# Optimization experiments

Measured on AMD Instinct MI355X. Metric: run time of the kernel, lower is better.

## Reference

```python
import jax, jax.numpy as jnp
import numpy as np

B, T, N, D = 4, 12, 10000, 2
E = 320000
H = 64          # encoder_embed_dim
K = 2           # Chebyshev diffusion steps
P = 1           # pred_node_dim
NPRED = 12      # n_pred


def _xavier(key, shape):
    fan_in, fan_out = shape[-2], shape[-1]
    limit = np.sqrt(6.0 / (fan_in + fan_out)).astype(np.float32)
    return jax.random.uniform(key, shape, jnp.float32, -limit, limit)


def setup_inputs() -> dict:
    key = jax.random.key(0)
    ks = jax.random.split(key, 8)
    x = jax.random.normal(ks[0], (B, T, N, D), jnp.float32)
    edge_index = jax.random.randint(ks[1], (2, E), 0, N, dtype=jnp.int64)
    # positive diffusion weights, scaled ~1/avg_degree for numerical sanity
    edge_attr = jax.random.uniform(ks[2], (E,), jnp.float32) * 0.03
    W0 = _xavier(ks[3], (K, D + H, H))   # layer 0: in = node_feat + H
    b0 = jnp.zeros((H,), jnp.float32)
    W1 = _xavier(ks[4], (K, 2 * H, H))   # layer 1: in = H + H
    b1 = jnp.zeros((H,), jnp.float32)
    Wp = _xavier(ks[5], (H, P))
    bp = jnp.zeros((P,), jnp.float32)
    return {"x": x, "edge_index": edge_index, "edge_attr": edge_attr,
            "W0": W0, "b0": b0, "W1": W1, "b1": b1, "Wp": Wp, "bp": bp}


def dcrnn_layer(x, h, src, dst, ew, W, b):
    # x: [B,N,Dx], h: [B,N,H]; inp: [B,N,C] with C = Dx + H
    inp = jnp.concatenate([x, h], axis=-1)
    out = jnp.einsum('bnc,co->bno', inp, W[0])
    Hc = inp
    for k in range(1, W.shape[0]):
        # propagate: message = norm * x_j (gather at src), scatter-add at dst
        msg = ew[None, :, None] * Hc[:, src]          # [B,E,C]
        Hc = jnp.zeros_like(Hc).at[:, dst].add(msg)   # [B,N,C]
        out = out + jnp.einsum('bnc,co->bno', Hc, W[k])
    return out + b


def reference(x, edge_index, edge_attr, W0, b0, W1, b1, Wp, bp):
    src, dst = edge_index[0], edge_index[1]
    Bs, Ts, Ns, _ = x.shape
    h0 = jnp.zeros((Bs, Ns, H), x.dtype)

    def step(h, x_t):
        # layer 0: input features + recurrent state
        h1 = jax.nn.relu(dcrnn_layer(x_t, h, src, dst, edge_attr, W0, b0))
        # layer 1: x_b = h_b after layer 0, so both halves are h1
        h2 = jax.nn.relu(dcrnn_layer(h1, h1, src, dst, edge_attr, W1, b1))
        return h2, None

    xs = jnp.swapaxes(x, 0, 1)  # [T,B,N,D]
    h, _ = jax.lax.scan(step, h0, xs)
    out = h @ Wp + bp                                  # [B,N,P]
    # unsqueeze(1).repeat(1, n_pred, 1, 1)
    return jnp.broadcast_to(out[:, None], (Bs, NPRED, Ns, out.shape[-1]))
```

## Files before the change

### kernel.cpp

```cpp
#include <hip/hip_runtime.h>

#define BB 4
#define TT 12
#define NN 10000
#define DD 2
#define EE 320000
#define HH 64
#define NPREDD 12
#define TD 24
#define CAP 512

typedef __attribute__((ext_vector_type(8))) short bf16x8;
typedef __attribute__((ext_vector_type(4))) float f32x4;
typedef unsigned short u16;

__device__ __forceinline__ unsigned int pack2(float lo, float hi) {
    unsigned int r;
    asm("v_cvt_pk_bf16_f32 %0, %1, %2" : "=v"(r) : "v"(lo), "v"(hi));
    return r;
}
__device__ __forceinline__ float b2f(u16 u) {
    return __uint_as_float(((unsigned)u) << 16);
}

__global__ void hist_kernel(const int* __restrict__ dstv, int* __restrict__ deg) {
    int e = blockIdx.x*256 + threadIdx.x;
    if (e < EE) atomicAdd(&deg[dstv[e]], 1);
}

__global__ void scan_kernel(const int* __restrict__ deg, int* __restrict__ row_ptr,
                            int* __restrict__ cursor) {
    __shared__ int part[1024];
    int tid = threadIdx.x;
    const int CH = 10;
    int start = tid*CH;
    int s = 0;
    if (start < NN)
        for (int i=0;i<CH;i++) s += deg[start+i];
    part[tid] = s;
    __syncthreads();
    if (tid == 0) {
        int acc = 0;
        for (int i=0;i<1024;i++){ int v=part[i]; part[i]=acc; acc+=v; }
        row_ptr[NN] = acc;
    }
    __syncthreads();
    if (start < NN) {
        int acc = part[tid];
        for (int i=0;i<CH;i++){ int idx=start+i; row_ptr[idx]=acc; cursor[idx]=acc; acc+=deg[idx]; }
    }
}

__global__ void fill_kernel(const int* __restrict__ srcv, const int* __restrict__ dstv,
                            const float* __restrict__ ew, int* __restrict__ cursor,
                            int2* __restrict__ csr) {
    int e = blockIdx.x*256 + threadIdx.x;
    if (e < EE) {
        int d = dstv[e];
        int pos = atomicAdd(&cursor[d], 1);
        csr[pos] = make_int2(srcv[e], __float_as_int(ew[e]));
    }
}

__global__ void transpose_x(const float* __restrict__ x, float* __restrict__ xTb) {
    int idx = blockIdx.x*256 + threadIdx.x;
    if (idx >= BB*TT*NN*DD) return;
    int d = idx & 1;
    int n = (idx >> 1) % NN;
    int t = (idx / (NN*DD)) % TT;
    int b = idx / (TT*NN*DD);
    xTb[((size_t)n*TD + (t*DD + d))*BB + b] = x[idx];
}

__global__ __launch_bounds__(256)
void ax_gather(const float* __restrict__ xTb, const int* __restrict__ row_ptr,
               const int2* __restrict__ csr, float* __restrict__ AXb) {
    int gw = (blockIdx.x*256 + threadIdx.x) >> 6;
    if (gw >= NN) return;
    int n = gw;
    int lane = threadIdx.x & 63;
    int half = lane >> 5;
    int c = lane & 31;
    float4 acc = {0.f,0.f,0.f,0.f};
    int e0 = row_ptr[n], e1 = row_ptr[n+1];
    for (int e = e0; e < e1; e += 8) {
        int ia = e + half, ib = e + 2 + half, ic = e + 4 + half, id = e + 6 + half;
        int2 ca = csr[ia]; int2 cb = csr[ib]; int2 cc = csr[ic]; int2 cd = csr[id];
        float wa = (ia < e1) ? __int_as_float(ca.y) : 0.f;
        float wb = (ib < e1) ? __int_as_float(cb.y) : 0.f;
        float wc = (ic < e1) ? __int_as_float(cc.y) : 0.f;
        float wd = (id < e1) ? __int_as_float(cd.y) : 0.f;
        const float4 va = *(const float4*)(xTb + (size_t)ca.x*(TD*BB) + c*4);
        const float4 vb = *(const float4*)(xTb + (size_t)cb.x*(TD*BB) + c*4);
        const float4 vc = *(const float4*)(xTb + (size_t)cc.x*(TD*BB) + c*4);
        const float4 vd = *(const float4*)(xTb + (size_t)cd.x*(TD*BB) + c*4);
        acc.x = fmaf(wa, va.x, acc.x); acc.y = fmaf(wa, va.y, acc.y);
        acc.z = fmaf(wa, va.z, acc.z); acc.w = fmaf(wa, va.w, acc.w);
        acc.x = fmaf(wb, vb.x, acc.x); acc.y = fmaf(wb, vb.y, acc.y);
        acc.z = fmaf(wb, vb.z, acc.z); acc.w = fmaf(wb, vb.w, acc.w);
        acc.x = fmaf(wc, vc.x, acc.x); acc.y = fmaf(wc, vc.y, acc.y);
        acc.z = fmaf(wc, vc.z, acc.z); acc.w = fmaf(wc, vc.w, acc.w);
        acc.x = fmaf(wd, vd.x, acc.x); acc.y = fmaf(wd, vd.y, acc.y);
        acc.z = fmaf(wd, vd.z, acc.z); acc.w = fmaf(wd, vd.w, acc.w);
    }
    acc.x += __shfl_xor(acc.x, 32); acc.y += __shfl_xor(acc.y, 32);
    acc.z += __shfl_xor(acc.z, 32); acc.w += __shfl_xor(acc.w, 32);
    if (lane < TD) *(float4*)(AXb + (size_t)n*(TD*BB) + lane*4) = acc;
}

__global__ void prep_wfrag(const float* __restrict__ W0, const float* __restrict__ W1,
                           unsigned short* __restrict__ wf0, unsigned short* __restrict__ wf1) {
    int tid = blockIdx.x*256 + threadIdx.x;
    if (tid >= 2560) return;
    int layer = tid / 1280;
    int r = tid % 1280;
    int lane = r & 63;
    int ctkt = r >> 6;
    int ct = ctkt / 5, kt = ctkt % 5;
    int c = ct*16 + (lane & 15);
    int k0 = kt*32 + (lane >> 4)*8;
    unsigned short* dst = (layer ? wf1 : wf0) + r*8;
    for (int j=0;j<8;j++) {
        int k = k0 + j;
        float w = 0.f;
        if (layer == 0) {
            if (k < 64)        w = W0[(2+k)*64 + c];
            else if (k < 128)  w = W0[4224 + (2+(k-64))*64 + c];
            else if (k == 128) w = W0[c];
            else if (k == 129) w = W0[64 + c];
            else if (k == 130) w = W0[4224 + c];
            else if (k == 131) w = W0[4224 + 64 + c];
        } else {
            if (k < 64)        w = W1[k*64 + c] + W1[(k+64)*64 + c];
            else if (k < 128)  w = W1[8192 + (k-64)*64 + c] + W1[8192 + k*64 + c];
        }
        unsigned int u = __float_as_uint(w);
        unsigned int rnd = (u + 0x7fffu + ((u >> 16) & 1u)) >> 16;
        dst[j] = (unsigned short)rnd;
    }
}

template<int L0>
__global__ __launch_bounds__(512)
void layer_kernel(const u16* __restrict__ h_in,
                  const float* __restrict__ x,
                  const float* __restrict__ AXb,
                  const unsigned short* __restrict__ wf,
                  const float* __restrict__ bias,
                  const int* __restrict__ row_ptr,
                  const int2* __restrict__ csr,
                  u16* __restrict__ h_out,
                  int t)
{
    __shared__ int2 sIdx[CAP];
    __shared__ unsigned short sA[32*168];

    int tid = threadIdx.x;
    int wave = tid >> 6, lane = tid & 63;
    int bq = lane >> 4, cq = lane & 15;

    int n0 = blockIdx.x * 8;
    int estart = row_ptr[n0];
    int eend   = row_ptr[n0 + 8];
    int cnt = eend - estart; if (cnt > CAP) cnt = CAP;

    {
        int2 v = make_int2(0, 0);
        if (tid < cnt) v = csr[estart + tid];
        sIdx[tid] = v;
    }

    int ct = wave & 3, rt = wave >> 2;
    const bf16x8* wfv = (const bf16x8*)wf;
    bf16x8 bfr[5];
    #pragma unroll
    for (int kt=0; kt<5; ++kt) bfr[kt] = wfv[(ct*5+kt)*64 + lane];
    float bv = bias[ct*16 + cq];

    int n = n0 + wave;
    int bseg = row_ptr[n] - estart;
    int eseg = row_ptr[n+1] - estart;

    ushort4 hv = *(const ushort4*)(h_in + ((size_t)n*BB + bq)*HH + cq*4);

    __syncthreads();

    float4 acc = {0.f,0.f,0.f,0.f};
    if (eseg <= cnt) {
        for (int e = bseg; e < eseg; e += 16) {
            #pragma unroll
            for (int u=0; u<16; ++u) {
                int idx = e + u;
                int2 cw = sIdx[idx & (CAP-1)];
                float w = (idx < eseg) ? __int_as_float(cw.y) : 0.f;
                ushort4 v = *(const ushort4*)(h_in + ((size_t)cw.x*BB + bq)*HH + cq*4);
                acc.x = fmaf(w, b2f(v.x), acc.x); acc.y = fmaf(w, b2f(v.y), acc.y);
                acc.z = fmaf(w, b2f(v.z), acc.z); acc.w = fmaf(w, b2f(v.w), acc.w);
            }
        }
    } else {
        for (int e = bseg; e < eseg; e += 16) {
            #pragma unroll
            for (int u=0; u<16; ++u) {
                int idx = e + u;
                int2 cw = (idx < eseg) ? csr[estart + idx] : make_int2(0,0);
                float w = (idx < eseg) ? __int_as_float(cw.y) : 0.f;
                ushort4 v = *(const ushort4*)(h_in + ((size_t)cw.x*BB + bq)*HH + cq*4);
                acc.x = fmaf(w, b2f(v.x), acc.x); acc.y = fmaf(w, b2f(v.y), acc.y);
                acc.z = fmaf(w, b2f(v.z), acc.z); acc.w = fmaf(w, b2f(v.w), acc.w);
            }
        }
    }

    int rowL = wave*4 + bq;
    *(ushort4*)&sA[rowL*168 + cq*4] = hv;
    { uint2 p; p.x = pack2(acc.x, acc.y); p.y = pack2(acc.z, acc.w);
      *(uint2*)&sA[rowL*168 + 64 + cq*4] = p; }
    if (cq == 0) {
        uint2 p;
        if (L0) {
            const float2 xv = *(const float2*)(x + (((size_t)bq*TT + t)*NN + n)*DD);
            float ax0 = AXb[(size_t)n*(TD*BB) + (2*t)*BB + bq];
            float ax1 = AXb[(size_t)n*(TD*BB) + (2*t+1)*BB + bq];
            p.x = pack2(xv.x, xv.y); p.y = pack2(ax0, ax1);
        } else {
            p.x = 0u; p.y = 0u;
        }
        *(uint2*)&sA[rowL*168 + 128] = p;
    } else if (cq < 8) {
        *(uint2*)&sA[rowL*168 + 132 + (cq-1)*4] = make_uint2(0u, 0u);
    }
    __syncthreads();

    f32x4 dacc = {0.f,0.f,0.f,0.f};
    #pragma unroll
    for (int kt=0; kt<5; ++kt) {
        bf16x8 a = *(const bf16x8*)&sA[(rt*16 + cq)*168 + kt*32 + bq*8];
        dacc = __builtin_amdgcn_mfma_f32_16x16x32_bf16(a, bfr[kt], dacc, 0, 0, 0);
    }
    #pragma unroll
    for (int i2=0;i2<4;i2++) {
        int r = rt*16 + bq*4 + i2;
        int nodeL = r >> 2, bo = r & 3;
        float v = fmaxf(dacc[i2] + bv, 0.f);
        unsigned p = pack2(v, v);
        h_out[((size_t)(n0 + nodeL)*BB + bo)*HH + ct*16 + cq] = (u16)p;
    }
}

__global__ void out_kernel(const u16* __restrict__ h, const float* __restrict__ Wp,
                           const float* __restrict__ bp, float* __restrict__ outp) {
    int g = blockIdx.x*256 + threadIdx.x;
    int wave = g >> 6, lane = g & 63;
    if (wave >= BB*NN) return;
    int b = wave / NN, n = wave - b*NN;
    float v = b2f(h[((size_t)n*BB + b)*HH + lane]) * Wp[lane];
    for (int off=32; off; off>>=1) v += __shfl_down(v, off);
    v = __shfl(v, 0) + bp[0];
    if (lane < NPREDD) outp[((size_t)b*NPREDD + lane)*NN + n] = v;
}

extern "C" void kernel_launch(void* const* d_in, const int* in_sizes, int n_in,
                              void* d_out, int out_size, void* d_ws, size_t ws_size,
                              hipStream_t stream) {
    const float* x   = (const float*)d_in[0];
    const int*   ei  = (const int*)d_in[1];
    const float* ew  = (const float*)d_in[2];
    const float* W0  = (const float*)d_in[3];
    const float* b0  = (const float*)d_in[4];
    const float* W1  = (const float*)d_in[5];
    const float* b1  = (const float*)d_in[6];
    const float* Wp  = (const float*)d_in[7];
    const float* bp  = (const float*)d_in[8];
    float* outp = (float*)d_out;

    char* ws = (char*)d_ws;
    size_t off = 0;
    auto alloc = [&](size_t bytes) { void* p = ws + off; off = (off + bytes + 255) & ~(size_t)255; return p; };
    u16* h      = (u16*)alloc((size_t)NN*BB*HH*2);
    u16* h1     = (u16*)alloc((size_t)NN*BB*HH*2);
    float* xTb  = (float*)alloc(((size_t)NN*TD*BB + 64)*4);
    float* AXb  = (float*)alloc((size_t)NN*TD*BB*4);
    unsigned short* wf0 = (unsigned short*)alloc(1280*8*2);
    unsigned short* wf1 = (unsigned short*)alloc(1280*8*2);
    int2*  csr  = (int2*)alloc(((size_t)EE + 16)*8);
    int* row_ptr= (int*)alloc((NN+1)*4);
    int* deg    = (int*)alloc(NN*4);
    int* cursor = (int*)alloc(NN*4);

    const int* srcv = ei;
    const int* dstv = ei + EE;

    hipMemsetAsync(deg, 0, NN*4, stream);
    hipMemsetAsync(h, 0, (size_t)NN*BB*HH*2, stream);
    hipMemsetAsync(csr + EE, 0, 16*8, stream);

    hist_kernel<<<(EE+255)/256, 256, 0, stream>>>(dstv, deg);
    scan_kernel<<<1, 1024, 0, stream>>>(deg, row_ptr, cursor);
    fill_kernel<<<(EE+255)/256, 256, 0, stream>>>(srcv, dstv, ew, cursor, csr);
    transpose_x<<<(BB*TT*NN*DD+255)/256, 256, 0, stream>>>(x, xTb);
    ax_gather<<<(NN*64+255)/256, 256, 0, stream>>>(xTb, row_ptr, csr, AXb);
    prep_wfrag<<<10, 256, 0, stream>>>(W0, W1, wf0, wf1);

    const int grid = 1250;
    for (int t=0; t<TT; ++t) {
        layer_kernel<1><<<grid, 512, 0, stream>>>(h,  x, AXb, wf0, b0, row_ptr, csr, h1, t);
        layer_kernel<0><<<grid, 512, 0, stream>>>(h1, nullptr, nullptr, wf1, b1, row_ptr, csr, h, 0);
    }
    out_kernel<<<(BB*NN*64+255)/256, 256, 0, stream>>>(h, Wp, bp, outp);
}
```

Measured before the change: 698.2 us.

## Replace per-step layer launches with one persistent cooperative kernel using grid sync

Replaces the 24 per-timestep layer launches and the output kernel with a single cooperative persistent kernel. It loops over time and both layers, separating phases with grid-wide barriers. Each block owns 40-node chunks for two batch elements, caches the chunk's CSR indices in shared memory once for all steps, and splits each node's edge gather across two half-waves. It also skips the gather at t=0 where the state is zero and fuses the output projection at the end. This removes launch overhead and repeated index loads, at the cost of grid-sync latency and a possible occupancy dependence: the grid is sized from a runtime occupancy query.

Result: slower. 1.662 ms (+138.1%).

```diff
diff --git a/kernel.cpp b/kernel.cpp
--- a/kernel.cpp
+++ b/kernel.cpp
@@ -1,4 +1,6 @@
 #include <hip/hip_runtime.h>
+#include <hip/hip_cooperative_groups.h>
+namespace cg = cooperative_groups;
 
 #define BB 4
 #define TT 12
@@ -8,7 +10,10 @@
 #define HH 64
 #define NPREDD 12
 #define TD 24
-#define CAP 512
+#define CHUNKS 250
+#define NPB 40
+#define NPW 5
+#define CAP 2048
 
 typedef __attribute__((ext_vector_type(8))) short bf16x8;
 typedef __attribute__((ext_vector_type(4))) float f32x4;
@@ -140,124 +145,171 @@
     }
 }
 
-template<int L0>
-__global__ __launch_bounds__(512)
-void layer_kernel(const u16* __restrict__ h_in,
-                  const float* __restrict__ x,
-                  const float* __restrict__ AXb,
-                  const unsigned short* __restrict__ wf,
-                  const float* __restrict__ bias,
-                  const int* __restrict__ row_ptr,
-                  const int2* __restrict__ csr,
-                  u16* __restrict__ h_out,
-                  int t)
+__global__ __launch_bounds__(512, 4)
+void persist_kernel(u16* __restrict__ hA, u16* __restrict__ hB,
+                    const float* __restrict__ x, const float* __restrict__ AXb,
+                    const unsigned short* __restrict__ wf0, const unsigned short* __restrict__ wf1,
+                    const float* __restrict__ b0, const float* __restrict__ b1,
+                    const int* __restrict__ row_ptr, const int2* __restrict__ csr,
+                    const float* __restrict__ Wp, const float* __restrict__ bp,
+                    float* __restrict__ outp)
 {
-    __shared__ int2 sIdx[CAP];
-    __shared__ unsigned short sA[32*168];
-
-    int tid = threadIdx.x;
-    int wave = tid >> 6, lane = tid & 63;
-    int bq = lane >> 4, cq = lane & 15;
-
-    int n0 = blockIdx.x * 8;
-    int estart = row_ptr[n0];
-    int eend   = row_ptr[n0 + 8];
-    int cnt = eend - estart; if (cnt > CAP) cnt = CAP;
-
-    {
-        int2 v = make_int2(0, 0);
-        if (tid < cnt) v = csr[estart + tid];
-        sIdx[tid] = v;
-    }
-
-    int ct = wave & 3, rt = wave >> 2;
-    const bf16x8* wfv = (const bf16x8*)wf;
-    bf16x8 bfr[5];
-    #pragma unroll
-    for (int kt=0; kt<5; ++kt) bfr[kt] = wfv[(ct*5+kt)*64 + lane];
-    float bv = bias[ct*16 + cq];
-
-    int n = n0 + wave;
-    int bseg = row_ptr[n] - estart;
-    int eseg = row_ptr[n+1] - estart;
-
-    ushort4 hv = *(const ushort4*)(h_in + ((size_t)n*BB + bq)*HH + cq*4);
-
+    __shared__ int2 sIdx[2][CAP];
+    __shared__ unsigned short sA[NPB*2*168];
+
+    cg::grid_group gg = cg::this_grid();
+
+    const int tid = threadIdx.x;
+    const int wave = tid >> 6, lane = tid & 63;
+    const int eh = lane >> 5, laneB = (lane >> 4) & 1, cq = lane & 15;
+    const int G = (int)gridDim.x;
+    const int bid = (int)blockIdx.x;
+    const int p = bid & 1;
+    const int ck0 = bid >> 1;
+    const int ck1 = ck0 + (G >> 1);
+    const int nck = (ck1 < CHUNKS) ? 2 : 1;
+    const int laneoff = ((p*2 + laneB)*HH + cq*4) * 2;
+
+    for (int s = 0; s < nck; ++s) {
+        int ck = (s == 0) ? ck0 : ck1;
+        int estart = row_ptr[ck*NPB];
+        int cnt = row_ptr[ck*NPB + NPB] - estart;
+        if (cnt > CAP) cnt = CAP;
+        for (int i = tid; i < CAP; i += 512) {
+            int2 v = make_int2(0, 0);
+            if (i < cnt) { int2 cw = csr[estart + i]; v = make_int2(cw.x << 9, cw.y); }
+            sIdx[s][i] = v;
+        }
+    }
     __syncthreads();
 
-    float4 acc = {0.f,0.f,0.f,0.f};
-    if (eseg <= cnt) {
-        for (int e = bseg; e < eseg; e += 16) {
-            #pragma unroll
-            for (int u=0; u<16; ++u) {
-                int idx = e + u;
-                int2 cw = sIdx[idx & (CAP-1)];
-                float w = (idx < eseg) ? __int_as_float(cw.y) : 0.f;
-                ushort4 v = *(const ushort4*)(h_in + ((size_t)cw.x*BB + bq)*HH + cq*4);
-                acc.x = fmaf(w, b2f(v.x), acc.x); acc.y = fmaf(w, b2f(v.y), acc.y);
-                acc.z = fmaf(w, b2f(v.z), acc.z); acc.w = fmaf(w, b2f(v.w), acc.w);
+    for (int t = 0; t < TT; ++t) {
+        for (int half = 0; half < 2; ++half) {
+            const int L0 = (half == 0);
+            const u16* hin = L0 ? hA : hB;
+            u16* hout = L0 ? hB : hA;
+            const unsigned short* wf = L0 ? wf0 : wf1;
+            const float* bias = L0 ? b0 : b1;
+
+            for (int s = 0; s < nck; ++s) {
+                int ck = (s == 0) ? ck0 : ck1;
+                int estart = row_ptr[ck*NPB];
+                int cntL = row_ptr[ck*NPB + NPB] - estart;
+                if (cntL > CAP) cntL = CAP;
+
+                for (int j = 0; j < NPW; ++j) {
+                    int n = ck*NPB + wave*NPW + j;
+                    int rowL = (wave*NPW + j)*2 + laneB;
+
+                    if (L0 && t == 0) {
+                        if (eh == 0) {
+                            *(uint2*)&sA[rowL*168 + cq*4] = make_uint2(0u,0u);
+                            *(uint2*)&sA[rowL*168 + 64 + cq*4] = make_uint2(0u,0u);
+                        }
+                    } else {
+                        int eb = row_ptr[n] - estart;
+                        int ee = row_ptr[n+1] - estart;
+                        ushort4 hv = make_ushort4(0,0,0,0);
+                        if (eh == 0)
+                            hv = *(const ushort4*)((const char*)hin + ((size_t)n << 9) + laneoff);
+                        float4 acc = {0.f,0.f,0.f,0.f};
+                        int tmax = (ee - eb + 31) >> 5;
+                        if (ee <= cntL) {
+                            for (int tt = 0; tt < tmax; ++tt) {
+                                int base = eb + (tt<<5) + eh;
+                                #pragma unroll
+                                for (int u = 0; u < 16; ++u) {
+                                    int idx = base + 2*u;
+                                    int2 ow = sIdx[s][idx & (CAP-1)];
+                                    float w = (idx < ee) ? __int_as_float(ow.y) : 0.f;
+                                    ushort4 v = *(const ushort4*)((const char*)hin + ow.x + laneoff);
+                                    acc.x = fmaf(w, b2f(v.x), acc.x);
+                                    acc.y = fmaf(w, b2f(v.y), acc.y);
+                                    acc.z = fmaf(w, b2f(v.z), acc.z);
+                                    acc.w = fmaf(w, b2f(v.w), acc.w);
+                                }
+                            }
+                        } else {
+                            for (int tt = 0; tt < tmax; ++tt) {
+                                int base = eb + (tt<<5) + eh;
+                                #pragma unroll
+                                for (int u = 0; u < 16; ++u) {
+                                    int idx = base + 2*u;
+                                    int2 cw = (idx < ee) ? csr[estart + idx] : make_int2(0,0);
+                                    float w = (idx < ee) ? __int_as_float(cw.y) : 0.f;
+                                    ushort4 v = *(const ushort4*)((const char*)hin + ((size_t)cw.x << 9) + laneoff);
+                                    acc.x = fmaf(w, b2f(v.x), acc.x);
+                                    acc.y = fmaf(w, b2f(v.y), acc.y);
+                                    acc.z = fmaf(w, b2f(v.z), acc.z);
+                                    acc.w = fmaf(w, b2f(v.w), acc.w);
+                                }
+                            }
+                        }
+                        acc.x += __shfl_xor(acc.x, 32); acc.y += __shfl_xor(acc.y, 32);
+                        acc.z += __shfl_xor(acc.z, 32); acc.w += __shfl_xor(acc.w, 32);
+                        if (eh == 0) {
+                            *(ushort4*)&sA[rowL*168 + cq*4] = hv;
+                            uint2 pk; pk.x = pack2(acc.x, acc.y); pk.y = pack2(acc.z, acc.w);
+                            *(uint2*)&sA[rowL*168 + 64 + cq*4] = pk;
+                        }
+                    }
+                    if (eh == 1) {
+                        if (cq == 0) {
+                            uint2 pk;
+                            if (L0) {
+                                int b = p*2 + laneB;
+                                const float2 xv = *(const float2*)(x + (((size_t)b*TT + t)*NN + n)*DD);
+                                float ax0 = AXb[(size_t)n*(TD*BB) + (2*t)*BB + b];
+                                float ax1 = AXb[(size_t)n*(TD*BB) + (2*t+1)*BB + b];
+                                pk.x = pack2(xv.x, xv.y); pk.y = pack2(ax0, ax1);
+                            } else { pk.x = 0u; pk.y = 0u; }
+                            *(uint2*)&sA[rowL*168 + 128] = pk;
+                        } else if (cq < 8) {
+                            *(uint2*)&sA[rowL*168 + 132 + (cq-1)*4] = make_uint2(0u,0u);
+                        }
+                    }
+                }
+                __syncthreads();
+
+                const bf16x8* wfv = (const bf16x8*)wf;
+                for (int tile = wave; tile < 20; tile += 8) {
+                    int mt = tile >> 2, ct = tile & 3;
+                    f32x4 dacc = {0.f,0.f,0.f,0.f};
+                    #pragma unroll
+                    for (int kt = 0; kt < 5; ++kt) {
+                        bf16x8 bfr = wfv[(ct*5 + kt)*64 + lane];
+                        bf16x8 a = *(const bf16x8*)&sA[(mt*16 + cq)*168 + kt*32 + (lane>>4)*8];
+                        dacc = __builtin_amdgcn_mfma_f32_16x16x32_bf16(a, bfr, dacc, 0, 0, 0);
+                    }
+                    float bv = bias[ct*16 + cq];
+                    #pragma unroll
+                    for (int i2 = 0; i2 < 4; ++i2) {
+                        int r = mt*16 + (lane>>4)*4 + i2;
+                        int n = ck*NPB + (r >> 1);
+                        int b = p*2 + (r & 1);
+                        float vv = fmaxf(dacc[i2] + bv, 0.f);
+                        unsigned pk = pack2(vv, vv);
+                        __builtin_nontemporal_store((u16)pk,
+                            hout + ((size_t)n*BB + b)*HH + ct*16 + cq);
+                    }
+                }
+                __syncthreads();
             }
+            if (!(t == TT-1 && half == 1)) gg.sync();
         }
-    } else {
-        for (int e = bseg; e < eseg; e += 16) {
-            #pragma unroll
-            for (int u=0; u<16; ++u) {
-                int idx = e + u;
-                int2 cw = (idx < eseg) ? csr[estart + idx] : make_int2(0,0);
-                float w = (idx < eseg) ? __int_as_float(cw.y) : 0.f;
-                ushort4 v = *(const ushort4*)(h_in + ((size_t)cw.x*BB + bq)*HH + cq*4);
-                acc.x = fmaf(w, b2f(v.x), acc.x); acc.y = fmaf(w, b2f(v.y), acc.y);
-                acc.z = fmaf(w, b2f(v.z), acc.z); acc.w = fmaf(w, b2f(v.w), acc.w);
-            }
+    }
+
+    for (int s = 0; s < nck; ++s) {
+        int ck = (s == 0) ? ck0 : ck1;
+        for (int r = wave; r < NPB*2; r += 8) {
+            int n = ck*NPB + (r >> 1);
+            int b = p*2 + (r & 1);
+            float v = b2f(hA[((size_t)n*BB + b)*HH + lane]) * Wp[lane];
+            for (int off = 32; off; off >>= 1) v += __shfl_down(v, off);
+            v = __shfl(v, 0) + bp[0];
+            if (lane < NPREDD) outp[((size_t)b*NPREDD + lane)*NN + n] = v;
         }
     }
-
-    int rowL = wave*4 + bq;
-    *(ushort4*)&sA[rowL*168 + cq*4] = hv;
-    { uint2 p; p.x = pack2(acc.x, acc.y); p.y = pack2(acc.z, acc.w);
-      *(uint2*)&sA[rowL*168 + 64 + cq*4] = p; }
-    if (cq == 0) {
-        uint2 p;
-        if (L0) {
-            const float2 xv = *(const float2*)(x + (((size_t)bq*TT + t)*NN + n)*DD);
-            float ax0 = AXb[(size_t)n*(TD*BB) + (2*t)*BB + bq];
-            float ax1 = AXb[(size_t)n*(TD*BB) + (2*t+1)*BB + bq];
-            p.x = pack2(xv.x, xv.y); p.y = pack2(ax0, ax1);
-        } else {
-            p.x = 0u; p.y = 0u;
-        }
-        *(uint2*)&sA[rowL*168 + 128] = p;
-    } else if (cq < 8) {
-        *(uint2*)&sA[rowL*168 + 132 + (cq-1)*4] = make_uint2(0u, 0u);
-    }
-    __syncthreads();
-
-    f32x4 dacc = {0.f,0.f,0.f,0.f};
-    #pragma unroll
-    for (int kt=0; kt<5; ++kt) {
-        bf16x8 a = *(const bf16x8*)&sA[(rt*16 + cq)*168 + kt*32 + bq*8];
-        dacc = __builtin_amdgcn_mfma_f32_16x16x32_bf16(a, bfr[kt], dacc, 0, 0, 0);
-    }
-    #pragma unroll
-    for (int i2=0;i2<4;i2++) {
-        int r = rt*16 + bq*4 + i2;
-        int nodeL = r >> 2, bo = r & 3;
-        float v = fmaxf(dacc[i2] + bv, 0.f);
-        unsigned p = pack2(v, v);
-        h_out[((size_t)(n0 + nodeL)*BB + bo)*HH + ct*16 + cq] = (u16)p;
-    }
-}
-
-__global__ void out_kernel(const u16* __restrict__ h, const float* __restrict__ Wp,
-                           const float* __restrict__ bp, float* __restrict__ outp) {
-    int g = blockIdx.x*256 + threadIdx.x;
-    int wave = g >> 6, lane = g & 63;
-    if (wave >= BB*NN) return;
-    int b = wave / NN, n = wave - b*NN;
-    float v = b2f(h[((size_t)n*BB + b)*HH + lane]) * Wp[lane];
-    for (int off=32; off; off>>=1) v += __shfl_down(v, off);
-    v = __shfl(v, 0) + bp[0];
-    if (lane < NPREDD) outp[((size_t)b*NPREDD + lane)*NN + n] = v;
 }
 
 extern "C" void kernel_launch(void* const* d_in, const int* in_sizes, int n_in,
@@ -302,10 +354,12 @@
     ax_gather<<<(NN*64+255)/256, 256, 0, stream>>>(xTb, row_ptr, csr, AXb);
     prep_wfrag<<<10, 256, 0, stream>>>(W0, W1, wf0, wf1);
 
-    const int grid = 1250;
-    for (int t=0; t<TT; ++t) {
-        layer_kernel<1><<<grid, 512, 0, stream>>>(h,  x, AXb, wf0, b0, row_ptr, csr, h1, t);
-        layer_kernel<0><<<grid, 512, 0, stream>>>(h1, nullptr, nullptr, wf1, b1, row_ptr, csr, h, 0);
-    }
-    out_kernel<<<(BB*NN*64+255)/256, 256, 0, stream>>>(h, Wp, bp, outp);
-}
+    int occ = 0;
+    hipOccupancyMaxActiveBlocksPerMultiprocessor(&occ, persist_kernel, 512, 0);
+    int Gr = (occ >= 2) ? 2*CHUNKS : CHUNKS;
+
+    void* kargs[] = { (void*)&h, (void*)&h1, (void*)&x, (void*)&AXb,
+                      (void*)&wf0, (void*)&wf1, (void*)&b0, (void*)&b1,
+                      (void*)&row_ptr, (void*)&csr, (void*)&Wp, (void*)&bp, (void*)&outp };
+    hipLaunchCooperativeKernel((void*)persist_kernel, dim3(Gr), dim3(512), kargs, 0, stream);
+}
```

## Split batch across block pairs, pre-shift gather offsets, skip zero-state first step

Applied to the files above, without the earlier changes.

Each block now handles 16 nodes and two of the four batch slices, with block pairs covering the full batch. The aim is more nodes per wave and edge indices staged once per 16 nodes, with source offsets pre-shifted to byte addresses to save per-edge address math. The t=0 layer-0 launch uses a Z=1 template that skips the neighbor gather and the h load, since the state is known to be zero, which also drops the memset of h. The CSR staging area doubles to 1024 entries, and each block pair now gathers the edge list twice, once for each batch half.

Result: no change. 708.1 us (+1.4%).

```diff
diff --git a/kernel.cpp b/kernel.cpp
--- a/kernel.cpp
+++ b/kernel.cpp
@@ -8,7 +8,7 @@
 #define HH 64
 #define NPREDD 12
 #define TD 24
-#define CAP 512
+#define CAP2 1024
 
 typedef __attribute__((ext_vector_type(8))) short bf16x8;
 typedef __attribute__((ext_vector_type(4))) float f32x4;
@@ -140,7 +140,7 @@
     }
 }
 
-template<int L0>
+template<int L0, int Z>
 __global__ __launch_bounds__(512)
 void layer_kernel(const u16* __restrict__ h_in,
                   const float* __restrict__ x,
@@ -152,81 +152,91 @@
                   u16* __restrict__ h_out,
                   int t)
 {
-    __shared__ int2 sIdx[CAP];
+    __shared__ int2 sIdx[CAP2];
     __shared__ unsigned short sA[32*168];
 
     int tid = threadIdx.x;
     int wave = tid >> 6, lane = tid & 63;
-    int bq = lane >> 4, cq = lane & 15;
-
-    int n0 = blockIdx.x * 8;
-    int estart = row_ptr[n0];
-    int eend   = row_ptr[n0 + 8];
-    int cnt = eend - estart; if (cnt > CAP) cnt = CAP;
-
-    {
-        int2 v = make_int2(0, 0);
-        if (tid < cnt) v = csr[estart + tid];
-        sIdx[tid] = v;
-    }
-
-    int ct = wave & 3, rt = wave >> 2;
+    int nsel = lane >> 5, laneB = (lane >> 4) & 1, cq = lane & 15;
+
+    int pair = blockIdx.x & 1;
+    int chunk = blockIdx.x >> 1;
+    int n0 = chunk * 16;
+    int b = pair*2 + laneB;
+    int laneoff = (b*HH + cq*4)*2;
+
+    int estart = 0, cnt = 0;
+    if (!Z) {
+        estart = row_ptr[n0];
+        cnt = row_ptr[n0 + 16] - estart;
+        int lim = cnt > CAP2 ? CAP2 : cnt;
+        for (int i = tid; i < CAP2; i += 512) {
+            int2 v = make_int2(0, 0);
+            if (i < lim) { int2 cw = csr[estart + i]; v = make_int2(cw.x << 9, cw.y); }
+            sIdx[i] = v;
+        }
+    }
+
+    int ct = wave & 3, mt = wave >> 2;
     const bf16x8* wfv = (const bf16x8*)wf;
     bf16x8 bfr[5];
     #pragma unroll
     for (int kt=0; kt<5; ++kt) bfr[kt] = wfv[(ct*5+kt)*64 + lane];
     float bv = bias[ct*16 + cq];
 
-    int n = n0 + wave;
-    int bseg = row_ptr[n] - estart;
-    int eseg = row_ptr[n+1] - estart;
-
-    ushort4 hv = *(const ushort4*)(h_in + ((size_t)n*BB + bq)*HH + cq*4);
-
-    __syncthreads();
-
+    int n = n0 + wave*2 + nsel;
+    int rowL = (wave*2 + nsel)*2 + laneB;
+
+    ushort4 hv = make_ushort4(0,0,0,0);
     float4 acc = {0.f,0.f,0.f,0.f};
-    if (eseg <= cnt) {
-        for (int e = bseg; e < eseg; e += 16) {
-            #pragma unroll
-            for (int u=0; u<16; ++u) {
-                int idx = e + u;
-                int2 cw = sIdx[idx & (CAP-1)];
-                float w = (idx < eseg) ? __int_as_float(cw.y) : 0.f;
-                ushort4 v = *(const ushort4*)(h_in + ((size_t)cw.x*BB + bq)*HH + cq*4);
-                acc.x = fmaf(w, b2f(v.x), acc.x); acc.y = fmaf(w, b2f(v.y), acc.y);
-                acc.z = fmaf(w, b2f(v.z), acc.z); acc.w = fmaf(w, b2f(v.w), acc.w);
+    if (!Z) {
+        int eb = row_ptr[n] - estart;
+        int ee = row_ptr[n+1] - estart;
+        hv = *(const ushort4*)((const char*)h_in + ((size_t)n << 9) + laneoff);
+        __syncthreads();
+        if (cnt <= CAP2) {
+            for (int e = eb; e < ee; e += 8) {
+                #pragma unroll
+                for (int u = 0; u < 8; ++u) {
+                    int idx = e + u;
+                    int2 ow = sIdx[idx & (CAP2-1)];
+                    float w = (idx < ee) ? __int_as_float(ow.y) : 0.f;
+                    ushort4 v = *(const ushort4*)((const char*)h_in + ow.x + laneoff);
+                    acc.x = fmaf(w, b2f(v.x), acc.x);
+                    acc.y = fmaf(w, b2f(v.y), acc.y);
+                    acc.z = fmaf(w, b2f(v.z), acc.z);
+                    acc.w = fmaf(w, b2f(v.w), acc.w);
+                }
+            }
+        } else {
+            for (int e = eb; e < ee; e += 8) {
+                #pragma unroll
+                for (int u = 0; u < 8; ++u) {
+                    int idx = e + u;
+                    int2 cw = (idx < ee) ? csr[estart + idx] : make_int2(0,0);
+                    float w = (idx < ee) ? __int_as_float(cw.y) : 0.f;
+                    ushort4 v = *(const ushort4*)((const char*)h_in + ((size_t)cw.x << 9) + laneoff);
+                    acc.x = fmaf(w, b2f(v.x), acc.x);
+                    acc.y = fmaf(w, b2f(v.y), acc.y);
+                    acc.z = fmaf(w, b2f(v.z), acc.z);
+                    acc.w = fmaf(w, b2f(v.w), acc.w);
+                }
             }
         }
-    } else {
-        for (int e = bseg; e < eseg; e += 16) {
-            #pragma unroll
-            for (int u=0; u<16; ++u) {
-                int idx = e + u;
-                int2 cw = (idx < eseg) ? csr[estart + idx] : make_int2(0,0);
-                float w = (idx < eseg) ? __int_as_float(cw.y) : 0.f;
-                ushort4 v = *(const ushort4*)(h_in + ((size_t)cw.x*BB + bq)*HH + cq*4);
-                acc.x = fmaf(w, b2f(v.x), acc.x); acc.y = fmaf(w, b2f(v.y), acc.y);
-                acc.z = fmaf(w, b2f(v.z), acc.z); acc.w = fmaf(w, b2f(v.w), acc.w);
-            }
-        }
-    }
-
-    int rowL = wave*4 + bq;
+    }
+
     *(ushort4*)&sA[rowL*168 + cq*4] = hv;
-    { uint2 p; p.x = pack2(acc.x, acc.y); p.y = pack2(acc.z, acc.w);
-      *(uint2*)&sA[rowL*168 + 64 + cq*4] = p; }
+    { uint2 pk; pk.x = pack2(acc.x, acc.y); pk.y = pack2(acc.z, acc.w);
+      *(uint2*)&sA[rowL*168 + 64 + cq*4] = pk; }
     if (cq == 0) {
-        uint2 p;
+        uint2 pk;
         if (L0) {
-            const float2 xv = *(const float2*)(x + (((size_t)bq*TT + t)*NN + n)*DD);
-            float ax0 = AXb[(size_t)n*(TD*BB) + (2*t)*BB + bq];
-            float ax1 = AXb[(size_t)n*(TD*BB) + (2*t+1)*BB + bq];
-            p.x = pack2(xv.x, xv.y); p.y = pack2(ax0, ax1);
-        } else {
-            p.x = 0u; p.y = 0u;
-        }
-        *(uint2*)&sA[rowL*168 + 128] = p;
+            const float2 xv = *(const float2*)(x + (((size_t)b*TT + t)*NN + n)*DD);
+            float ax0 = AXb[(size_t)n*(TD*BB) + (2*t)*BB + b];
+            float ax1 = AXb[(size_t)n*(TD*BB) + (2*t+1)*BB + b];
+            pk.x = pack2(xv.x, xv.y); pk.y = pack2(ax0, ax1);
+        } else { pk.x = 0u; pk.y = 0u; }
+        *(uint2*)&sA[rowL*168 + 128] = pk;
     } else if (cq < 8) {
         *(uint2*)&sA[rowL*168 + 132 + (cq-1)*4] = make_uint2(0u, 0u);
     }
@@ -235,16 +245,16 @@
     f32x4 dacc = {0.f,0.f,0.f,0.f};
     #pragma unroll
     for (int kt=0; kt<5; ++kt) {
-        bf16x8 a = *(const bf16x8*)&sA[(rt*16 + cq)*168 + kt*32 + bq*8];
+        bf16x8 a = *(const bf16x8*)&sA[(mt*16 + cq)*168 + kt*32 + (lane>>4)*8];
         dacc = __builtin_amdgcn_mfma_f32_16x16x32_bf16(a, bfr[kt], dacc, 0, 0, 0);
     }
     #pragma unroll
     for (int i2=0;i2<4;i2++) {
-        int r = rt*16 + bq*4 + i2;
-        int nodeL = r >> 2, bo = r & 3;
-        float v = fmaxf(dacc[i2] + bv, 0.f);
-        unsigned p = pack2(v, v);
-        h_out[((size_t)(n0 + nodeL)*BB + bo)*HH + ct*16 + cq] = (u16)p;
+        int r = mt*16 + (lane>>4)*4 + i2;
+        int nodeL = r >> 1, bo = pair*2 + (r & 1);
+        float vv = fmaxf(dacc[i2] + bv, 0.f);
+        unsigned pk = pack2(vv, vv);
+        h_out[((size_t)(n0 + nodeL)*BB + bo)*HH + ct*16 + cq] = (u16)pk;
     }
 }
 
@@ -292,7 +302,6 @@
     const int* dstv = ei + EE;
 
     hipMemsetAsync(deg, 0, NN*4, stream);
-    hipMemsetAsync(h, 0, (size_t)NN*BB*HH*2, stream);
     hipMemsetAsync(csr + EE, 0, 16*8, stream);
 
     hist_kernel<<<(EE+255)/256, 256, 0, stream>>>(dstv, deg);
@@ -303,9 +312,11 @@
     prep_wfrag<<<10, 256, 0, stream>>>(W0, W1, wf0, wf1);
 
     const int grid = 1250;
-    for (int t=0; t<TT; ++t) {
-        layer_kernel<1><<<grid, 512, 0, stream>>>(h,  x, AXb, wf0, b0, row_ptr, csr, h1, t);
-        layer_kernel<0><<<grid, 512, 0, stream>>>(h1, nullptr, nullptr, wf1, b1, row_ptr, csr, h, 0);
+    layer_kernel<1,1><<<grid, 512, 0, stream>>>(h,  x, AXb, wf0, b0, row_ptr, csr, h1, 0);
+    layer_kernel<0,0><<<grid, 512, 0, stream>>>(h1, nullptr, nullptr, wf1, b1, row_ptr, csr, h, 0);
+    for (int t=1; t<TT; ++t) {
+        layer_kernel<1,0><<<grid, 512, 0, stream>>>(h,  x, AXb, wf0, b0, row_ptr, csr, h1, t);
+        layer_kernel<0,0><<<grid, 512, 0, stream>>>(h1, nullptr, nullptr, wf1, b1, row_ptr, csr, h, 0);
     }
     out_kernel<<<(BB*NN*64+255)/256, 256, 0, stream>>>(h, Wp, bp, outp);
 }
```
